# Performance work log

Measured on AMD Instinct MI355X. Metric: run time of the kernel, lower is better.

## Reference

```python
import jax, jax.numpy as jnp
import numpy as np

B = 1024
FEATS = [("sirna_gibbs_energy", 19), ("pssm_score", 1), ("gc_sterch", 1), ("sirna_second_percent", 2), ("sirna_second_energy", 2), ("tri_nt_percent", 64), ("di_nt_percent", 16), ("single_nt_percent", 4), ("gc_content", 1)]
DFF = 2048  # torch TransformerEncoderLayer default dim_feedforward


def _posenc(S, d):
    pos = jnp.arange(S, dtype=jnp.float32)[:, None]
    div = jnp.exp(jnp.arange(0, d, 2, dtype=jnp.float32) * (-np.log(10000.0) / d))
    pe = jnp.zeros((S, d), jnp.float32)
    pe = pe.at[:, 0::2].set(jnp.sin(pos * div))
    pe = pe.at[:, 1::2].set(jnp.cos(pos * div))
    return pe


def _ln(x, g, b):
    m = x.mean(-1, keepdims=True)
    v = ((x - m) ** 2).mean(-1, keepdims=True)
    return (x - m) * jax.lax.rsqrt(v + 1e-5) * g + b


def _encoder_layer(x, qkv_w, qkv_b, ow, ob, f1w, f1b, f2w, f2b, g1, b1, g2, b2, nhead):
    Bx, S, d = x.shape
    dh = d // nhead
    qkv = jnp.einsum('bsd,ed->bse', x, qkv_w) + qkv_b  # [B,S,3d]
    q, k, v = jnp.split(qkv, 3, axis=-1)
    sh = lambda t: t.reshape(Bx, S, nhead, dh).transpose(0, 2, 1, 3)  # [B,h,S,dh]
    q, k, v = sh(q), sh(k), sh(v)
    att = jax.nn.softmax(jnp.einsum('bhqd,bhkd->bhqk', q, k) / np.sqrt(dh).astype(np.float32), axis=-1)
    o = jnp.einsum('bhqk,bhkd->bhqd', att, v).transpose(0, 2, 1, 3).reshape(Bx, S, d)
    o = o @ ow.T + ob
    x = _ln(x + o, g1, b1)  # post-norm (norm_first=False default)
    h = jax.nn.relu(x @ f1w.T + f1b) @ f2w.T + f2b
    return _ln(x + h, g2, b2)


def _encoder(x, qkv_w, qkv_b, ow, ob, f1w, f1b, f2w, f2b, g1, b1, g2, b2, nhead):
    for i in range(qkv_w.shape[0]):
        x = _encoder_layer(x, qkv_w[i], qkv_b[i], ow[i], ob[i], f1w[i], f1b[i], f2w[i], f2b[i], g1[i], b1[i], g2[i], b2[i], nhead)
    return x


def setup_inputs():
    key = jax.random.key(0)
    ks = iter(jax.random.split(key, 128))
    inp = {}
    inp['rnafm_encode'] = jax.random.normal(next(ks), (B, 21, 640), jnp.float32)
    inp['rnafm_encode_mrna'] = jax.random.normal(next(ks), (B, 59, 640), jnp.float32)
    for name, n in FEATS:
        inp[name] = jax.random.normal(next(ks), (B, n, 1), jnp.float32)

    def xav(shape):
        fan_out, fan_in = shape[-2], shape[-1]
        std = np.sqrt(2.0 / (fan_in + fan_out)).astype(np.float32)
        return jax.random.normal(next(ks), shape, jnp.float32) * std

    def enc_params(prefix, L, d):
        inp[prefix + '_qkv_w'] = xav((L, 3 * d, d))
        inp[prefix + '_qkv_b'] = jnp.zeros((L, 3 * d), jnp.float32)
        inp[prefix + '_ow'] = xav((L, d, d))
        inp[prefix + '_ob'] = jnp.zeros((L, d), jnp.float32)
        inp[prefix + '_f1w'] = xav((L, DFF, d))
        inp[prefix + '_f1b'] = jnp.zeros((L, DFF), jnp.float32)
        inp[prefix + '_f2w'] = xav((L, d, DFF))
        inp[prefix + '_f2b'] = jnp.zeros((L, d), jnp.float32)
        inp[prefix + '_g1'] = jnp.ones((L, d), jnp.float32)
        inp[prefix + '_b1'] = jnp.zeros((L, d), jnp.float32)
        inp[prefix + '_g2'] = jnp.ones((L, d), jnp.float32)
        inp[prefix + '_b2'] = jnp.zeros((L, d), jnp.float32)

    inp['xmap1_w'] = xav((16, 640)); inp['xmap1_b'] = jnp.zeros(16, jnp.float32)
    enc_params('enc1', 4, 16)
    inp['ymap1_w'] = xav((4, 16)); inp['ymap1_b'] = jnp.zeros(4, jnp.float32)
    inp['xmap2_w'] = xav((8, 640)); inp['xmap2_b'] = jnp.zeros(8, jnp.float32)
    enc_params('enc2', 2, 8)
    inp['ymap2_w'] = xav((1, 8)); inp['ymap2_b'] = jnp.zeros(1, jnp.float32)
    inp['bn_g'] = jnp.ones(253, jnp.float32); inp['bn_b'] = jnp.zeros(253, jnp.float32)
    inp['d1w'] = xav((256, 253)); inp['d1b'] = jnp.zeros(256, jnp.float32)
    inp['d2w'] = xav((64, 256)); inp['d2b'] = jnp.zeros(64, jnp.float32)
    inp['d3w'] = xav((16, 64)); inp['d3b'] = jnp.zeros(16, jnp.float32)
    inp['d4w'] = xav((1, 16)); inp['d4b'] = jnp.zeros(1, jnp.float32)
    return inp


def _forward(rnafm_encode, rnafm_encode_mrna, feats,
             xmap1_w, xmap1_b, enc1, ymap1_w, ymap1_b,
             xmap2_w, xmap2_b, enc2, ymap2_w, ymap2_b,
             bn_g, bn_b, d1w, d1b, d2w, d2b, d3w, d3b, d4w, d4b):
    # siRNA branch: [B,21,640] -> [B,21,16] -> encoder(4 layers, 2 heads) -> [B,21,4]
    x = rnafm_encode @ xmap1_w.T + xmap1_b
    x = x + _posenc(21, 16)
    x = _encoder(x, *enc1, nhead=2)
    as_att = (x @ ymap1_w.T + ymap1_b).reshape(x.shape[0], -1)  # [B,84]
    # mRNA branch: [B,59,640] -> [B,59,8] -> encoder(2 layers, 1 head) -> [B,59,1]
    y = rnafm_encode_mrna @ xmap2_w.T + xmap2_b
    y = y + _posenc(59, 8)
    y = _encoder(y, *enc2, nhead=1)
    mrna_att = (y @ ymap2_w.T + ymap2_b).reshape(y.shape[0], -1)  # [B,59]
    other = jnp.concatenate([f[..., 0] for f in feats], axis=1)  # [B,110]
    cat = jnp.concatenate([as_att, mrna_att, other], axis=1)  # [B,253]
    # BatchNorm1d in eval mode (running_mean=0, running_var=1, eps=1e-5)
    h = cat * jax.lax.rsqrt(jnp.float32(1.0 + 1e-5)) * bn_g + bn_b
    h = jax.nn.leaky_relu(h @ d1w.T + d1b, 0.01)
    h = jax.nn.leaky_relu(h @ d2w.T + d2b, 0.01)
    h = jax.nn.leaky_relu(h @ d3w.T + d3b, 0.01)
    out = jax.nn.sigmoid(h @ d4w.T + d4b)
    return out[:, 0]


def reference(rnafm_encode, rnafm_encode_mrna, sirna_gibbs_energy, pssm_score, gc_sterch,
              sirna_second_percent, sirna_second_energy, tri_nt_percent, di_nt_percent,
              single_nt_percent, gc_content,
              xmap1_w, xmap1_b,
              enc1_qkv_w, enc1_qkv_b, enc1_ow, enc1_ob, enc1_f1w, enc1_f1b, enc1_f2w, enc1_f2b,
              enc1_g1, enc1_b1, enc1_g2, enc1_b2,
              ymap1_w, ymap1_b,
              xmap2_w, xmap2_b,
              enc2_qkv_w, enc2_qkv_b, enc2_ow, enc2_ob, enc2_f1w, enc2_f1b, enc2_f2w, enc2_f2b,
              enc2_g1, enc2_b1, enc2_g2, enc2_b2,
              ymap2_w, ymap2_b,
              bn_g, bn_b, d1w, d1b, d2w, d2b, d3w, d3b, d4w, d4b):
    feats = (sirna_gibbs_energy, pssm_score, gc_sterch, sirna_second_percent,
             sirna_second_energy, tri_nt_percent, di_nt_percent, single_nt_percent, gc_content)
    enc1 = (enc1_qkv_w, enc1_qkv_b, enc1_ow, enc1_ob, enc1_f1w, enc1_f1b, enc1_f2w, enc1_f2b,
            enc1_g1, enc1_b1, enc1_g2, enc1_b2)
    enc2 = (enc2_qkv_w, enc2_qkv_b, enc2_ow, enc2_ob, enc2_f1w, enc2_f1b, enc2_f2w, enc2_f2b,
            enc2_g1, enc2_b1, enc2_g2, enc2_b2)
    return _forward(rnafm_encode, rnafm_encode_mrna, feats,
                    xmap1_w, xmap1_b, enc1, ymap1_w, ymap1_b,
                    xmap2_w, xmap2_b, enc2, ymap2_w, ymap2_b,
                    bn_g, bn_b, d1w, d1b, d2w, d2b, d3w, d3b, d4w, d4b)
```

## Files before the change

kernel.cpp:

```cpp
#include <hip/hip_runtime.h>
#include <math.h>

#define NB 1024

typedef __bf16 mbf8 __attribute__((ext_vector_type(8)));
typedef float  mf4  __attribute__((ext_vector_type(4)));

union Pk { __bf16 h[4]; uint2 u2; };

__device__ __forceinline__ mf4 mfma16(mbf8 a, mbf8 b, mf4 c) {
  return __builtin_amdgcn_mfma_f32_16x16x32_bf16(a, b, c, 0, 0, 0);
}

__device__ __forceinline__ mbf8 ld_frag_f32(const float* p) {
  float4 u0 = *(const float4*)p;
  float4 u1 = *(const float4*)(p + 4);
  mbf8 v;
  v[0]=(__bf16)u0.x; v[1]=(__bf16)u0.y; v[2]=(__bf16)u0.z; v[3]=(__bf16)u0.w;
  v[4]=(__bf16)u1.x; v[5]=(__bf16)u1.y; v[6]=(__bf16)u1.z; v[7]=(__bf16)u1.w;
  return v;
}

__device__ __forceinline__ mbf8 ld_frag_f32_scaled(const float* p, float s) {
  float4 u0 = *(const float4*)p;
  float4 u1 = *(const float4*)(p + 4);
  mbf8 v;
  v[0]=(__bf16)(u0.x*s); v[1]=(__bf16)(u0.y*s); v[2]=(__bf16)(u0.z*s); v[3]=(__bf16)(u0.w*s);
  v[4]=(__bf16)(u1.x*s); v[5]=(__bf16)(u1.y*s); v[6]=(__bf16)(u1.z*s); v[7]=(__bf16)(u1.w*s);
  return v;
}

__device__ __forceinline__ mbf8 zero8() {
  mbf8 v;
  #pragma unroll
  for (int q = 0; q < 8; ++q) v[q] = (__bf16)0.f;
  return v;
}

__global__ __launch_bounds__(256) void prep_kernel(
    const float* __restrict__ xw1, const float* __restrict__ f1w1, const float* __restrict__ f2w1,
    const float* __restrict__ xw2, const float* __restrict__ f1w2, const float* __restrict__ f2w2,
    const float* __restrict__ d1w, const float* __restrict__ d2w, const float* __restrict__ d3w,
    __bf16* __restrict__ out)
{
  int idx = blockIdx.x * 256 + threadIdx.x;
  if (idx >= 693248) return;
  int which, local;
  if (idx < 10240)       { which = 0; local = idx; }
  else if (idx < 272384) { which = 1; local = idx - 10240; }
  else if (idx < 403456) { which = 2; local = idx - 272384; }
  else if (idx < 413696) { which = 3; local = idx - 403456; }
  else if (idx < 544768) { which = 4; local = idx - 413696; }
  else if (idx < 610304) { which = 5; local = idx - 544768; }
  else if (idx < 675840) { which = 6; local = idx - 610304; }
  else if (idx < 692224) { which = 7; local = idx - 675840; }
  else                   { which = 8; local = idx - 692224; }
  int tile = local >> 9, r = local & 511, lane = r >> 3, j = r & 7;
  int quad = lane >> 4, lm = lane & 15, khi = quad * 8 + j;
  float val = 0.f;
  switch (which) {
    case 0: { int k = tile*32 + khi; val = xw1[lm*640 + k]; } break;
    case 1: { int L = tile >> 7, nt = tile & 127, n = nt*16 + lm;
              val = (khi < 16) ? f1w1[(L*2048 + n)*16 + khi] : 0.f; } break;
    case 2: { int L = tile >> 6, ks = tile & 63, k = ks*32 + khi;
              val = f2w1[(L*16 + lm)*2048 + k]; } break;
    case 3: { int k = tile*32 + khi; val = (lm < 8) ? xw2[lm*640 + k] : 0.f; } break;
    case 4: { int L = tile >> 7, nt = tile & 127, n = nt*16 + lm;
              val = (khi < 8) ? f1w2[(L*2048 + n)*8 + khi] : 0.f; } break;
    case 5: { int L = tile >> 6, ks = tile & 63, k = ks*32 + khi;
              val = (lm < 8) ? f2w2[(L*8 + lm)*2048 + k] : 0.f; } break;
    case 6: { int nt = tile >> 3, ks = tile & 7, k = ks*32 + khi;
              val = (k < 253) ? d1w[(nt*16 + lm)*253 + k] : 0.f; } break;
    case 7: { int nt = tile >> 3, ks = tile & 7, k = ks*32 + khi;
              val = d2w[(nt*16 + lm)*256 + k]; } break;
    default:{ int ks = tile, k = ks*32 + khi;
              val = d3w[lm*64 + k]; } break;
  }
  out[idx] = (__bf16)val;
}

__device__ __forceinline__ void run_b1(int b, float* smem,
    const float* __restrict__ inp, const float* __restrict__ xb,
    const float* __restrict__ qw, const float* __restrict__ qb,
    const float* __restrict__ ow, const float* __restrict__ ob,
    const float* __restrict__ f1b, const float* __restrict__ f2b,
    const float* __restrict__ g1w, const float* __restrict__ b1w,
    const float* __restrict__ g2w, const float* __restrict__ b2w,
    const float* __restrict__ ymw, const float* __restrict__ ymb,
    const __bf16* __restrict__ xwB, const __bf16* __restrict__ w1B,
    const __bf16* __restrict__ w2B, float* __restrict__ outp)
{
  float* xs   = smem;
  float* ao   = smem + 420;
  float* pool = smem + 840;

  const int tid = threadIdx.x;
  const int w = tid >> 6, lane = tid & 63, quad = lane >> 4, lm = lane & 15;
  float* qkv = pool;
  __bf16* pbuf = (__bf16*)(pool + 1092);
  __bf16* hbuf = (__bf16*)pool;
  float* red = pool;
  const float* Ain = inp + (size_t)b * 21 * 640;

  mf4 pc0 = {0.f,0.f,0.f,0.f}, pc1 = {0.f,0.f,0.f,0.f};
  for (int i = 0; i < 5; ++i) {
    int ks = w*5 + i;
    mbf8 bv = *(const mbf8*)(xwB + (ks*64 + lane)*8);
    #pragma unroll
    for (int mt = 0; mt < 2; ++mt) {
      int row = mt*16 + lm; row = row > 20 ? 20 : row;
      mbf8 av = ld_frag_f32(Ain + row*640 + ks*32 + quad*8);
      if (mt == 0) pc0 = mfma16(av, bv, pc0); else pc1 = mfma16(av, bv, pc1);
    }
  }
  #pragma unroll
  for (int r = 0; r < 4; ++r) {
    red[((w*2+0)*16 + quad*4 + r)*17 + lm] = pc0[r];
    red[((w*2+1)*16 + quad*4 + r)*17 + lm] = pc1[r];
  }
  __syncthreads();
  {
    const float lf = -logf(10000.0f) / 16.0f;
    for (int idx = tid; idx < 336; idx += 256) {
      int t = idx >> 4, i = idx & 15, mt = t >> 4, tl = t & 15;
      float s = red[((0+mt)*16+tl)*17+i] + red[((2+mt)*16+tl)*17+i]
              + red[((4+mt)*16+tl)*17+i] + red[((6+mt)*16+tl)*17+i];
      float freq = expf((float)((i>>1)*2) * lf);
      float pe = (i & 1) ? cosf((float)t * freq) : sinf((float)t * freq);
      xs[t*20 + i] = s + xb[i] + pe;
    }
  }
  __syncthreads();

  for (int L = 0; L < 4; ++L) {
    for (int idx = tid; idx < 1008; idx += 256) {
      int s = idx / 48, e = idx % 48;
      const float* wr = qw + (L*48 + e)*16;
      float a = qb[L*48 + e];
      #pragma unroll
      for (int k = 0; k < 16; ++k) a += xs[s*20+k] * wr[k];
      qkv[s*52 + e] = a;
    }
    __syncthreads();

    {
      int h = w >> 1, mt = w & 1;
      __bf16* pb = pbuf + w*640;
      int tokq = mt*16 + lm; tokq = tokq > 20 ? 20 : tokq;
      mbf8 qf = zero8();
      if (quad == 0) qf = ld_frag_f32_scaled(qkv + tokq*52 + h*8, 0.35355339059327373f);
      float scr[2][4];
      #pragma unroll
      for (int nt = 0; nt < 2; ++nt) {
        int key = nt*16 + lm; key = key > 20 ? 20 : key;
        mbf8 kf = zero8();
        if (quad == 0) kf = ld_frag_f32(qkv + key*52 + 16 + h*8);
        mf4 z = {0.f,0.f,0.f,0.f};
        mf4 c = mfma16(qf, kf, z);
        int col = nt*16 + lm;
        #pragma unroll
        for (int r = 0; r < 4; ++r) scr[nt][r] = (col < 21) ? c[r] : -1e30f;
      }
      #pragma unroll
      for (int r = 0; r < 4; ++r) {
        float m = fmaxf(scr[0][r], scr[1][r]);
        m = fmaxf(m, __shfl_xor(m, 1)); m = fmaxf(m, __shfl_xor(m, 2));
        m = fmaxf(m, __shfl_xor(m, 4)); m = fmaxf(m, __shfl_xor(m, 8));
        float e0 = __expf(scr[0][r] - m), e1 = __expf(scr[1][r] - m);
        float s = e0 + e1;
        s += __shfl_xor(s, 1); s += __shfl_xor(s, 2);
        s += __shfl_xor(s, 4); s += __shfl_xor(s, 8);
        float inv = 1.f / s;
        scr[0][r] = e0 * inv; scr[1][r] = e1 * inv;
      }
      #pragma unroll
      for (int nt = 0; nt < 2; ++nt)
        #pragma unroll
        for (int r = 0; r < 4; ++r)
          pb[(quad*4 + r)*40 + nt*16 + lm] = (__bf16)scr[nt][r];
      mbf8 pf = *(const mbf8*)(pb + lm*40 + quad*8);
      mbf8 vf = zero8();
      #pragma unroll
      for (int j = 0; j < 8; ++j) {
        int k = quad*8 + j;
        vf[j] = (__bf16)((lm < 8 && k < 21) ? qkv[k*52 + 32 + h*8 + lm] : 0.f);
      }
      mf4 z = {0.f,0.f,0.f,0.f};
      mf4 c = mfma16(pf, vf, z);
      #pragma unroll
      for (int r = 0; r < 4; ++r) {
        int tok = mt*16 + quad*4 + r;
        if (tok < 21 && lm < 8) ao[tok*20 + h*8 + lm] = c[r];
      }
    }
    __syncthreads();

    for (int idx = tid; idx < 336; idx += 256) {
      int s = idx >> 4, i = idx & 15;
      const float* wr = ow + (L*16 + i)*16;
      float a = ob[L*16 + i];
      #pragma unroll
      for (int c = 0; c < 16; ++c) a += ao[s*20 + c] * wr[c];
      float v = xs[s*20 + i] + a;
      float m = v;
      m += __shfl_xor(m, 1); m += __shfl_xor(m, 2);
      m += __shfl_xor(m, 4); m += __shfl_xor(m, 8);
      m *= (1.f/16.f);
      float d = v - m;
      float va = d*d;
      va += __shfl_xor(va, 1); va += __shfl_xor(va, 2);
      va += __shfl_xor(va, 4); va += __shfl_xor(va, 8);
      va *= (1.f/16.f);
      xs[s*20 + i] = d * rsqrtf(va + 1e-5f) * g1w[L*16+i] + b1w[L*16+i];
    }
    __syncthreads();

    mbf8 xf0 = zero8(), xf1 = zero8();
    if (quad < 2) {
      int t0 = lm;
      int t1 = 16 + lm; if (t1 > 20) t1 = 20;
      xf0 = ld_frag_f32(xs + t0*20 + quad*8);
      xf1 = ld_frag_f32(xs + t1*20 + quad*8);
    }
    mf4 of0 = {0.f,0.f,0.f,0.f}, of1 = {0.f,0.f,0.f,0.f};
    const __bf16* w1L = w1B + (size_t)L*128*512;
    const __bf16* w2L = w2B + (size_t)L*64*512;
    const float* f1bL = f1b + L*2048;
    for (int ci = 0; ci < 8; ++ci) {
      #pragma unroll
      for (int u = 0; u < 4; ++u) {
        int ut = ci*16 + w*4 + u;
        mbf8 wa = *(const mbf8*)(w1L + (ut*64 + lane)*8);
        float4 bia = *(const float4*)(f1bL + ut*16 + quad*4);
        mf4 z = {0.f,0.f,0.f,0.f};
        mf4 c0 = mfma16(wa, xf0, z);
        mf4 c1 = mfma16(wa, xf1, z);
        Pk p0, p1;
        p0.h[0]=(__bf16)fmaxf(c0[0]+bia.x,0.f); p0.h[1]=(__bf16)fmaxf(c0[1]+bia.y,0.f);
        p0.h[2]=(__bf16)fmaxf(c0[2]+bia.z,0.f); p0.h[3]=(__bf16)fmaxf(c0[3]+bia.w,0.f);
        p1.h[0]=(__bf16)fmaxf(c1[0]+bia.x,0.f); p1.h[1]=(__bf16)fmaxf(c1[1]+bia.y,0.f);
        p1.h[2]=(__bf16)fmaxf(c1[2]+bia.z,0.f); p1.h[3]=(__bf16)fmaxf(c1[3]+bia.w,0.f);
        int colb = (ut & 15)*16 + quad*4;
        *(uint2*)(hbuf + lm*264 + colb)        = p0.u2;
        *(uint2*)(hbuf + (16 + lm)*264 + colb) = p1.u2;
      }
      #pragma unroll
      for (int kk = 0; kk < 2; ++kk) {
        int ksl = w*2 + kk;
        mbf8 wb = *(const mbf8*)(w2L + ((ci*8 + ksl)*64 + lane)*8);
        mbf8 a0 = *(const mbf8*)(hbuf + lm*264 + ksl*32 + quad*8);
        mbf8 a1 = *(const mbf8*)(hbuf + (16 + lm)*264 + ksl*32 + quad*8);
        of0 = mfma16(a0, wb, of0);
        of1 = mfma16(a1, wb, of1);
      }
    }
    __syncthreads();
    #pragma unroll
    for (int r = 0; r < 4; ++r) {
      red[((w*2+0)*16 + quad*4 + r)*17 + lm] = of0[r];
      red[((w*2+1)*16 + quad*4 + r)*17 + lm] = of1[r];
    }
    __syncthreads();
    for (int idx = tid; idx < 336; idx += 256) {
      int t = idx >> 4, i = idx & 15, mt = t >> 4, tl = t & 15;
      float s = red[((0+mt)*16+tl)*17+i] + red[((2+mt)*16+tl)*17+i]
              + red[((4+mt)*16+tl)*17+i] + red[((6+mt)*16+tl)*17+i];
      float v = xs[t*20 + i] + s + f2b[L*16 + i];
      float m = v;
      m += __shfl_xor(m, 1); m += __shfl_xor(m, 2);
      m += __shfl_xor(m, 4); m += __shfl_xor(m, 8);
      m *= (1.f/16.f);
      float d = v - m;
      float va = d*d;
      va += __shfl_xor(va, 1); va += __shfl_xor(va, 2);
      va += __shfl_xor(va, 4); va += __shfl_xor(va, 8);
      va *= (1.f/16.f);
      xs[t*20 + i] = d * rsqrtf(va + 1e-5f) * g2w[L*16+i] + b2w[L*16+i];
    }
    __syncthreads();
  }

  for (int idx = tid; idx < 84; idx += 256) {
    int s = idx >> 2, j = idx & 3;
    float a = ymb[j];
    #pragma unroll
    for (int k = 0; k < 16; ++k) a += xs[s*20 + k] * ymw[j*16 + k];
    outp[(size_t)b*84 + idx] = a;
  }
}

__device__ __forceinline__ void run_b2(int b, float* smem,
    const float* __restrict__ inp, const float* __restrict__ xb,
    const float* __restrict__ qw, const float* __restrict__ qb,
    const float* __restrict__ ow, const float* __restrict__ ob,
    const float* __restrict__ f1b, const float* __restrict__ f2b,
    const float* __restrict__ g1w, const float* __restrict__ b1w,
    const float* __restrict__ g2w, const float* __restrict__ b2w,
    const float* __restrict__ ymw, const float* __restrict__ ymb,
    const __bf16* __restrict__ xwB, const __bf16* __restrict__ w1B,
    const __bf16* __restrict__ w2B, float* __restrict__ outp)
{
  float* xs   = smem;
  float* ao   = smem + 708;
  float* pool = smem + 1416;

  const int tid = threadIdx.x;
  const int w = tid >> 6, lane = tid & 63, quad = lane >> 4, lm = lane & 15;
  float* qkv = pool;
  __bf16* pbuf = (__bf16*)(pool + 1652);
  __bf16* hbuf = (__bf16*)pool;
  float* red = pool;
  const float* Ain = inp + (size_t)b * 59 * 640;

  mf4 pc[4];
  #pragma unroll
  for (int mt = 0; mt < 4; ++mt) { mf4 z = {0.f,0.f,0.f,0.f}; pc[mt] = z; }
  for (int i = 0; i < 5; ++i) {
    int ks = w*5 + i;
    mbf8 bv = *(const mbf8*)(xwB + (ks*64 + lane)*8);
    #pragma unroll
    for (int mt = 0; mt < 4; ++mt) {
      int row = mt*16 + lm; row = row > 58 ? 58 : row;
      mbf8 av = ld_frag_f32(Ain + row*640 + ks*32 + quad*8);
      pc[mt] = mfma16(av, bv, pc[mt]);
    }
  }
  #pragma unroll
  for (int mt = 0; mt < 4; ++mt)
    #pragma unroll
    for (int r = 0; r < 4; ++r)
      red[((w*4+mt)*16 + quad*4 + r)*17 + lm] = pc[mt][r];
  __syncthreads();
  {
    const float lf = -logf(10000.0f) / 8.0f;
    for (int idx = tid; idx < 472; idx += 256) {
      int t = idx >> 3, i = idx & 7, mt = t >> 4, tl = t & 15;
      float s = red[((0*4+mt)*16+tl)*17+i] + red[((1*4+mt)*16+tl)*17+i]
              + red[((2*4+mt)*16+tl)*17+i] + red[((3*4+mt)*16+tl)*17+i];
      float freq = expf((float)((i>>1)*2) * lf);
      float pe = (i & 1) ? cosf((float)t * freq) : sinf((float)t * freq);
      xs[t*12 + i] = s + xb[i] + pe;
    }
  }
  __syncthreads();

  for (int L = 0; L < 2; ++L) {
    for (int idx = tid; idx < 1416; idx += 256) {
      int s = idx / 24, e = idx % 24;
      const float* wr = qw + (L*24 + e)*8;
      float a = qb[L*24 + e];
      #pragma unroll
      for (int k = 0; k < 8; ++k) a += xs[s*12+k] * wr[k];
      qkv[s*28 + e] = a;
    }
    __syncthreads();

    {
      __bf16* pb = pbuf + w*1152;
      int tokq = w*16 + lm; tokq = tokq > 58 ? 58 : tokq;
      mbf8 qf = zero8();
      if (quad == 0) qf = ld_frag_f32_scaled(qkv + tokq*28, 0.35355339059327373f);
      float scr[4][4];
      #pragma unroll
      for (int nt = 0; nt < 4; ++nt) {
        int key = nt*16 + lm; key = key > 58 ? 58 : key;
        mbf8 kf = zero8();
        if (quad == 0) kf = ld_frag_f32(qkv + key*28 + 8);
        mf4 z = {0.f,0.f,0.f,0.f};
        mf4 c = mfma16(qf, kf, z);
        int col = nt*16 + lm;
        #pragma unroll
        for (int r = 0; r < 4; ++r) scr[nt][r] = (col < 59) ? c[r] : -1e30f;
      }
      #pragma unroll
      for (int r = 0; r < 4; ++r) {
        float m = fmaxf(fmaxf(scr[0][r], scr[1][r]), fmaxf(scr[2][r], scr[3][r]));
        m = fmaxf(m, __shfl_xor(m, 1)); m = fmaxf(m, __shfl_xor(m, 2));
        m = fmaxf(m, __shfl_xor(m, 4)); m = fmaxf(m, __shfl_xor(m, 8));
        float e0 = __expf(scr[0][r] - m), e1 = __expf(scr[1][r] - m);
        float e2 = __expf(scr[2][r] - m), e3 = __expf(scr[3][r] - m);
        float s = (e0 + e1) + (e2 + e3);
        s += __shfl_xor(s, 1); s += __shfl_xor(s, 2);
        s += __shfl_xor(s, 4); s += __shfl_xor(s, 8);
        float inv = 1.f / s;
        scr[0][r] = e0 * inv; scr[1][r] = e1 * inv;
        scr[2][r] = e2 * inv; scr[3][r] = e3 * inv;
      }
      #pragma unroll
      for (int nt = 0; nt < 4; ++nt)
        #pragma unroll
        for (int r = 0; r < 4; ++r)
          pb[(quad*4 + r)*72 + nt*16 + lm] = (__bf16)scr[nt][r];
      mf4 acc = {0.f,0.f,0.f,0.f};
      #pragma unroll
      for (int kk = 0; kk < 2; ++kk) {
        mbf8 pf = *(const mbf8*)(pb + lm*72 + kk*32 + quad*8);
        mbf8 vf = zero8();
        #pragma unroll
        for (int j = 0; j < 8; ++j) {
          int k = kk*32 + quad*8 + j;
          vf[j] = (__bf16)((lm < 8 && k < 59) ? qkv[k*28 + 16 + lm] : 0.f);
        }
        acc = mfma16(pf, vf, acc);
      }
      #pragma unroll
      for (int r = 0; r < 4; ++r) {
        int tok = w*16 + quad*4 + r;
        if (tok < 59 && lm < 8) ao[tok*12 + lm] = acc[r];
      }
    }
    __syncthreads();

    for (int idx = tid; idx < 472; idx += 256) {
      int s = idx >> 3, i = idx & 7;
      const float* wr = ow + (L*8 + i)*8;
      float a = ob[L*8 + i];
      #pragma unroll
      for (int c = 0; c < 8; ++c) a += ao[s*12 + c] * wr[c];
      float v = xs[s*12 + i] + a;
      float m = v;
      m += __shfl_xor(m, 1); m += __shfl_xor(m, 2); m += __shfl_xor(m, 4);
      m *= 0.125f;
      float d = v - m;
      float va = d*d;
      va += __shfl_xor(va, 1); va += __shfl_xor(va, 2); va += __shfl_xor(va, 4);
      va *= 0.125f;
      xs[s*12 + i] = d * rsqrtf(va + 1e-5f) * g1w[L*8+i] + b1w[L*8+i];
    }
    __syncthreads();

    mbf8 xf[4];
    #pragma unroll
    for (int tt = 0; tt < 4; ++tt) {
      xf[tt] = zero8();
      if (quad == 0) {
        int tok = tt*16 + lm; if (tok > 58) tok = 58;
        xf[tt] = ld_frag_f32(xs + tok*12);
      }
    }
    mf4 of[4];
    #pragma unroll
    for (int mt = 0; mt < 4; ++mt) { mf4 z = {0.f,0.f,0.f,0.f}; of[mt] = z; }
    const __bf16* w1L = w1B + (size_t)L*128*512;
    const __bf16* w2L = w2B + (size_t)L*64*512;
    const float* f1bL = f1b + L*2048;
    for (int ci = 0; ci < 16; ++ci) {
      #pragma unroll
      for (int u = 0; u < 2; ++u) {
        int ut = ci*8 + w*2 + u;
        mbf8 wa = *(const mbf8*)(w1L + (ut*64 + lane)*8);
        float4 bia = *(const float4*)(f1bL + ut*16 + quad*4);
        int colb = (ut & 7)*16 + quad*4;
        #pragma unroll
        for (int tt = 0; tt < 4; ++tt) {
          mf4 z = {0.f,0.f,0.f,0.f};
          mf4 c = mfma16(wa, xf[tt], z);
          Pk p;
          p.h[0]=(__bf16)fmaxf(c[0]+bia.x,0.f); p.h[1]=(__bf16)fmaxf(c[1]+bia.y,0.f);
          p.h[2]=(__bf16)fmaxf(c[2]+bia.z,0.f); p.h[3]=(__bf16)fmaxf(c[3]+bia.w,0.f);
          *(uint2*)(hbuf + (tt*16 + lm)*136 + colb) = p.u2;
        }
      }
      {
        mbf8 wb = *(const mbf8*)(w2L + ((ci*4 + w)*64 + lane)*8);
        #pragma unroll
        for (int mt = 0; mt < 4; ++mt) {
          mbf8 ah = *(const mbf8*)(hbuf + (mt*16 + lm)*136 + w*32 + quad*8);
          of[mt] = mfma16(ah, wb, of[mt]);
        }
      }
    }
    __syncthreads();
    #pragma unroll
    for (int mt = 0; mt < 4; ++mt)
      #pragma unroll
      for (int r = 0; r < 4; ++r)
        red[((w*4+mt)*16 + quad*4 + r)*17 + lm] = of[mt][r];
    __syncthreads();
    for (int idx = tid; idx < 472; idx += 256) {
      int t = idx >> 3, i = idx & 7, mt = t >> 4, tl = t & 15;
      float s = red[((0*4+mt)*16+tl)*17+i] + red[((1*4+mt)*16+tl)*17+i]
              + red[((2*4+mt)*16+tl)*17+i] + red[((3*4+mt)*16+tl)*17+i];
      float v = xs[t*12 + i] + s + f2b[L*8 + i];
      float m = v;
      m += __shfl_xor(m, 1); m += __shfl_xor(m, 2); m += __shfl_xor(m, 4);
      m *= 0.125f;
      float d = v - m;
      float va = d*d;
      va += __shfl_xor(va, 1); va += __shfl_xor(va, 2); va += __shfl_xor(va, 4);
      va *= 0.125f;
      xs[t*12 + i] = d * rsqrtf(va + 1e-5f) * g2w[L*8+i] + b2w[L*8+i];
    }
    __syncthreads();
  }

  for (int s = tid; s < 59; s += 256) {
    float a = ymb[0];
    #pragma unroll
    for (int k = 0; k < 8; ++k) a += xs[s*12 + k] * ymw[k];
    outp[(size_t)b*59 + s] = a;
  }
}

__global__ __launch_bounds__(256) void enc_kernel(
    const float* __restrict__ inp1, const float* __restrict__ inp2,
    const float* __restrict__ xb1,
    const float* __restrict__ qw1, const float* __restrict__ qb1,
    const float* __restrict__ ow1, const float* __restrict__ ob1,
    const float* __restrict__ f1b1, const float* __restrict__ f2b1,
    const float* __restrict__ g1w1, const float* __restrict__ b1w1,
    const float* __restrict__ g2w1, const float* __restrict__ b2w1,
    const float* __restrict__ ymw1, const float* __restrict__ ymb1,
    const __bf16* __restrict__ xw1B, const __bf16* __restrict__ w1B1,
    const __bf16* __restrict__ w2B1,
    const float* __restrict__ xb2,
    const float* __restrict__ qw2, const float* __restrict__ qb2,
    const float* __restrict__ ow2, const float* __restrict__ ob2,
    const float* __restrict__ f1b2, const float* __restrict__ f2b2,
    const float* __restrict__ g1w2, const float* __restrict__ b1w2,
    const float* __restrict__ g2w2, const float* __restrict__ b2w2,
    const float* __restrict__ ymw2, const float* __restrict__ ymb2,
    const __bf16* __restrict__ xw2B, const __bf16* __restrict__ w1B2,
    const __bf16* __restrict__ w2B2,
    float* __restrict__ as_att, float* __restrict__ mrna)
{
  __shared__ __align__(16) float smem[5792];
  int bid = blockIdx.x;
  int b = bid >> 1;
  if ((bid & 1) == 0) {
    run_b1(b, smem, inp1, xb1, qw1, qb1, ow1, ob1, f1b1, f2b1,
           g1w1, b1w1, g2w1, b2w1, ymw1, ymb1, xw1B, w1B1, w2B1, as_att);
  } else {
    run_b2(b, smem, inp2, xb2, qw2, qb2, ow2, ob2, f1b2, f2b2,
           g1w2, b1w2, g2w2, b2w2, ymw2, ymb2, xw2B, w1B2, w2B2, mrna);
  }
}

__global__ __launch_bounds__(256) void mlp_kernel(
    const float* __restrict__ as_att, const float* __restrict__ mrna,
    const float* __restrict__ f_gibbs, const float* __restrict__ f_pssm,
    const float* __restrict__ f_gcs, const float* __restrict__ f_ssp,
    const float* __restrict__ f_sse, const float* __restrict__ f_tri,
    const float* __restrict__ f_di, const float* __restrict__ f_sgl,
    const float* __restrict__ f_gc,
    const float* __restrict__ bn_g, const float* __restrict__ bn_b,
    const float* __restrict__ d1b, const float* __restrict__ d2b,
    const float* __restrict__ d3b,
    const float* __restrict__ d4w, const float* __restrict__ d4b,
    const __bf16* __restrict__ d1B, const __bf16* __restrict__ d2B,
    const __bf16* __restrict__ d3B,
    float* __restrict__ outp)
{
  __shared__ __align__(16) float cat[16*268];
  __shared__ __align__(16) float h1[16*268];
  __shared__ __align__(16) float h2[16*68];
  __shared__ __align__(16) float h3[16*17];
  const int tid = threadIdx.x;
  const int bs  = blockIdx.x * 16;
  const int w = tid >> 6, lane = tid & 63, quad = lane >> 4, lm = lane & 15;
  const float bnscale = rsqrtf(1.0f + 1e-5f);

  for (int g = 0; g < 16; ++g) {
    int smp = bs + g;
    for (int j = tid; j < 253; j += 256) {
      float v;
      if (j < 84)       v = as_att[(size_t)smp*84 + j];
      else if (j < 143) v = mrna[(size_t)smp*59 + (j - 84)];
      else {
        int j2 = j - 143;
        if (j2 < 19)       v = f_gibbs[smp*19 + j2];
        else if (j2 < 20)  v = f_pssm[smp];
        else if (j2 < 21)  v = f_gcs[smp];
        else if (j2 < 23)  v = f_ssp[smp*2 + (j2-21)];
        else if (j2 < 25)  v = f_sse[smp*2 + (j2-23)];
        else if (j2 < 89)  v = f_tri[smp*64 + (j2-25)];
        else if (j2 < 105) v = f_di[smp*16 + (j2-89)];
        else if (j2 < 109) v = f_sgl[smp*4 + (j2-105)];
        else               v = f_gc[smp];
      }
      cat[g*268 + j] = v * bnscale * bn_g[j] + bn_b[j];
    }
  }
  if (tid < 48) { int g = tid / 3; cat[g*268 + 253 + tid % 3] = 0.f; }
  __syncthreads();

  {
    mf4 acc[4];
    #pragma unroll
    for (int q = 0; q < 4; ++q) { mf4 z = {0.f,0.f,0.f,0.f}; acc[q] = z; }
    for (int ks = 0; ks < 8; ++ks) {
      mbf8 af = ld_frag_f32(cat + lm*268 + ks*32 + quad*8);
      #pragma unroll
      for (int nt4 = 0; nt4 < 4; ++nt4) {
        int nt = w*4 + nt4;
        mbf8 bf = *(const mbf8*)(d1B + ((nt*8 + ks)*64 + lane)*8);
        acc[nt4] = mfma16(af, bf, acc[nt4]);
      }
    }
    #pragma unroll
    for (int nt4 = 0; nt4 < 4; ++nt4) {
      int n = (w*4 + nt4)*16 + lm;
      float bb = d1b[n];
      #pragma unroll
      for (int r = 0; r < 4; ++r) {
        float a = acc[nt4][r] + bb;
        h1[(quad*4 + r)*268 + n] = (a > 0.f) ? a : 0.01f * a;
      }
    }
  }
  __syncthreads();

  {
    mf4 acc = {0.f,0.f,0.f,0.f};
    for (int ks = 0; ks < 8; ++ks) {
      mbf8 af = ld_frag_f32(h1 + lm*268 + ks*32 + quad*8);
      mbf8 bf = *(const mbf8*)(d2B + ((w*8 + ks)*64 + lane)*8);
      acc = mfma16(af, bf, acc);
    }
    int n = w*16 + lm;
    float bb = d2b[n];
    #pragma unroll
    for (int r = 0; r < 4; ++r) {
      float a = acc[r] + bb;
      h2[(quad*4 + r)*68 + n] = (a > 0.f) ? a : 0.01f * a;
    }
  }
  __syncthreads();

  if (w == 0) {
    mf4 acc = {0.f,0.f,0.f,0.f};
    #pragma unroll
    for (int ks = 0; ks < 2; ++ks) {
      mbf8 af = ld_frag_f32(h2 + lm*68 + ks*32 + quad*8);
      mbf8 bf = *(const mbf8*)(d3B + (ks*64 + lane)*8);
      acc = mfma16(af, bf, acc);
    }
    float bb = d3b[lm];
    #pragma unroll
    for (int r = 0; r < 4; ++r) {
      float a = acc[r] + bb;
      h3[(quad*4 + r)*17 + lm] = (a > 0.f) ? a : 0.01f * a;
    }
  }
  __syncthreads();

  if (tid < 16) {
    float a = d4b[0];
    #pragma unroll
    for (int j = 0; j < 16; ++j) a += h3[tid*17 + j] * d4w[j];
    outp[bs + tid] = 1.f / (1.f + __expf(-a));
  }
}

extern "C" void kernel_launch(void* const* d_in, const int* in_sizes, int n_in,
                              void* d_out, int out_size, void* d_ws, size_t ws_size,
                              hipStream_t stream) {
  const float* rnafm   = (const float*)d_in[0];
  const float* rnafm_m = (const float*)d_in[1];
  const float* f_gibbs = (const float*)d_in[2];
  const float* f_pssm  = (const float*)d_in[3];
  const float* f_gcs   = (const float*)d_in[4];
  const float* f_ssp   = (const float*)d_in[5];
  const float* f_sse   = (const float*)d_in[6];
  const float* f_tri   = (const float*)d_in[7];
  const float* f_di    = (const float*)d_in[8];
  const float* f_sgl   = (const float*)d_in[9];
  const float* f_gc    = (const float*)d_in[10];
  const float* xmap1_w = (const float*)d_in[11];
  const float* xmap1_b = (const float*)d_in[12];
  const float* e1_qw   = (const float*)d_in[13];
  const float* e1_qb   = (const float*)d_in[14];
  const float* e1_ow   = (const float*)d_in[15];
  const float* e1_ob   = (const float*)d_in[16];
  const float* e1_f1w  = (const float*)d_in[17];
  const float* e1_f1b  = (const float*)d_in[18];
  const float* e1_f2w  = (const float*)d_in[19];
  const float* e1_f2b  = (const float*)d_in[20];
  const float* e1_g1   = (const float*)d_in[21];
  const float* e1_b1   = (const float*)d_in[22];
  const float* e1_g2   = (const float*)d_in[23];
  const float* e1_b2   = (const float*)d_in[24];
  const float* ymap1_w = (const float*)d_in[25];
  const float* ymap1_b = (const float*)d_in[26];
  const float* xmap2_w = (const float*)d_in[27];
  const float* xmap2_b = (const float*)d_in[28];
  const float* e2_qw   = (const float*)d_in[29];
  const float* e2_qb   = (const float*)d_in[30];
  const float* e2_ow   = (const float*)d_in[31];
  const float* e2_ob   = (const float*)d_in[32];
  const float* e2_f1w  = (const float*)d_in[33];
  const float* e2_f1b  = (const float*)d_in[34];
  const float* e2_f2w  = (const float*)d_in[35];
  const float* e2_f2b  = (const float*)d_in[36];
  const float* e2_g1   = (const float*)d_in[37];
  const float* e2_b1   = (const float*)d_in[38];
  const float* e2_g2   = (const float*)d_in[39];
  const float* e2_b2   = (const float*)d_in[40];
  const float* ymap2_w = (const float*)d_in[41];
  const float* ymap2_b = (const float*)d_in[42];
  const float* bn_g    = (const float*)d_in[43];
  const float* bn_b    = (const float*)d_in[44];
  const float* d1w     = (const float*)d_in[45];
  const float* d1b     = (const float*)d_in[46];
  const float* d2w     = (const float*)d_in[47];
  const float* d2b     = (const float*)d_in[48];
  const float* d3w     = (const float*)d_in[49];
  const float* d3b     = (const float*)d_in[50];
  const float* d4w     = (const float*)d_in[51];
  const float* d4b     = (const float*)d_in[52];

  float* as_att = (float*)d_ws;
  float* mrna   = (float*)((char*)d_ws + (size_t)NB*84*4);
  __bf16* bfb   = (__bf16*)((char*)d_ws + 585728);
  __bf16* xw1B  = bfb;
  __bf16* w1B1  = bfb + 10240;
  __bf16* w2B1  = bfb + 272384;
  __bf16* xw2B  = bfb + 403456;
  __bf16* w1B2  = bfb + 413696;
  __bf16* w2B2  = bfb + 544768;
  __bf16* d1B   = bfb + 610304;
  __bf16* d2B   = bfb + 675840;
  __bf16* d3B   = bfb + 692224;
  float* outp   = (float*)d_out;

  prep_kernel<<<2708, 256, 0, stream>>>(xmap1_w, e1_f1w, e1_f2w, xmap2_w, e2_f1w, e2_f2w,
                                        d1w, d2w, d3w, bfb);

  enc_kernel<<<2*NB, 256, 0, stream>>>(rnafm, rnafm_m,
      xmap1_b, e1_qw, e1_qb, e1_ow, e1_ob, e1_f1b, e1_f2b,
      e1_g1, e1_b1, e1_g2, e1_b2, ymap1_w, ymap1_b, xw1B, w1B1, w2B1,
      xmap2_b, e2_qw, e2_qb, e2_ow, e2_ob, e2_f1b, e2_f2b,
      e2_g1, e2_b1, e2_g2, e2_b2, ymap2_w, ymap2_b, xw2B, w1B2, w2B2,
      as_att, mrna);

  mlp_kernel<<<64, 256, 0, stream>>>(as_att, mrna,
      f_gibbs, f_pssm, f_gcs, f_ssp, f_sse, f_tri, f_di, f_sgl, f_gc,
      bn_g, bn_b, d1b, d2b, d3b, d4w, d4b, d1B, d2B, d3B, outp);
}
```

Before: 516.6 us.

## Use MFMA for QKV and output projections and pad FFN hidden buffer stride

```diff
diff --git a/kernel.cpp b/kernel.cpp
--- a/kernel.cpp
+++ b/kernel.cpp
@@ -41,10 +41,12 @@
     const float* __restrict__ xw1, const float* __restrict__ f1w1, const float* __restrict__ f2w1,
     const float* __restrict__ xw2, const float* __restrict__ f1w2, const float* __restrict__ f2w2,
     const float* __restrict__ d1w, const float* __restrict__ d2w, const float* __restrict__ d3w,
+    const float* __restrict__ qw1, const float* __restrict__ ow1,
+    const float* __restrict__ qw2, const float* __restrict__ ow2,
     __bf16* __restrict__ out)
 {
   int idx = blockIdx.x * 256 + threadIdx.x;
-  if (idx >= 693248) return;
+  if (idx >= 704512) return;
   int which, local;
   if (idx < 10240)       { which = 0; local = idx; }
   else if (idx < 272384) { which = 1; local = idx - 10240; }
@@ -54,7 +56,11 @@
   else if (idx < 610304) { which = 5; local = idx - 544768; }
   else if (idx < 675840) { which = 6; local = idx - 610304; }
   else if (idx < 692224) { which = 7; local = idx - 675840; }
-  else                   { which = 8; local = idx - 692224; }
+  else if (idx < 693248) { which = 8; local = idx - 692224; }
+  else if (idx < 699392) { which = 9; local = idx - 693248; }
+  else if (idx < 701440) { which = 10; local = idx - 699392; }
+  else if (idx < 703488) { which = 11; local = idx - 701440; }
+  else                   { which = 12; local = idx - 703488; }
   int tile = local >> 9, r = local & 511, lane = r >> 3, j = r & 7;
   int quad = lane >> 4, lm = lane & 15, khi = quad * 8 + j;
   float val = 0.f;
@@ -73,22 +79,30 @@
               val = (k < 253) ? d1w[(nt*16 + lm)*253 + k] : 0.f; } break;
     case 7: { int nt = tile >> 3, ks = tile & 7, k = ks*32 + khi;
               val = d2w[(nt*16 + lm)*256 + k]; } break;
-    default:{ int ks = tile, k = ks*32 + khi;
+    case 8: { int ks = tile, k = ks*32 + khi;
               val = d3w[lm*64 + k]; } break;
+    case 9: { int L = tile / 3, nt = tile % 3, n = nt*16 + lm;
+              val = (khi < 16) ? qw1[(L*48 + n)*16 + khi] : 0.f; } break;
+    case 10:{ int L = tile;
+              val = (khi < 16) ? ow1[(L*16 + lm)*16 + khi] : 0.f; } break;
+    case 11:{ int L = tile >> 1, nt = tile & 1, n = nt*16 + lm;
+              val = (n < 24 && khi < 8) ? qw2[(L*24 + n)*8 + khi] : 0.f; } break;
+    default:{ int L = tile;
+              val = (lm < 8 && khi < 8) ? ow2[(L*8 + lm)*8 + khi] : 0.f; } break;
   }
   out[idx] = (__bf16)val;
 }
 
 __device__ __forceinline__ void run_b1(int b, float* smem,
     const float* __restrict__ inp, const float* __restrict__ xb,
-    const float* __restrict__ qw, const float* __restrict__ qb,
-    const float* __restrict__ ow, const float* __restrict__ ob,
+    const float* __restrict__ qb, const float* __restrict__ ob,
     const float* __restrict__ f1b, const float* __restrict__ f2b,
     const float* __restrict__ g1w, const float* __restrict__ b1w,
     const float* __restrict__ g2w, const float* __restrict__ b2w,
     const float* __restrict__ ymw, const float* __restrict__ ymb,
     const __bf16* __restrict__ xwB, const __bf16* __restrict__ w1B,
-    const __bf16* __restrict__ w2B, float* __restrict__ outp)
+    const __bf16* __restrict__ w2B, const __bf16* __restrict__ qkvB,
+    const __bf16* __restrict__ owB, float* __restrict__ outp)
 {
   float* xs   = smem;
   float* ao   = smem + 420;
@@ -133,13 +147,28 @@
   __syncthreads();
 
   for (int L = 0; L < 4; ++L) {
-    for (int idx = tid; idx < 1008; idx += 256) {
-      int s = idx / 48, e = idx % 48;
-      const float* wr = qw + (L*48 + e)*16;
-      float a = qb[L*48 + e];
-      #pragma unroll
-      for (int k = 0; k < 16; ++k) a += xs[s*20+k] * wr[k];
-      qkv[s*52 + e] = a;
+    {
+      int mt = w & 1;
+      mbf8 axf = zero8();
+      if (quad < 2) {
+        int t = mt*16 + lm; if (t > 20) t = 20;
+        axf = ld_frag_f32(xs + t*20 + quad*8);
+      }
+      const float* qbL = qb + L*48;
+      int npass = (w < 2) ? 2 : 1;
+      for (int pass = 0; pass < npass; ++pass) {
+        int nt = (w < 2) ? pass*2 : 1;
+        mbf8 bf = *(const mbf8*)(qkvB + ((L*3 + nt)*512) + lane*8);
+        mf4 z = {0.f,0.f,0.f,0.f};
+        mf4 c = mfma16(axf, bf, z);
+        int e = nt*16 + lm;
+        float bias = qbL[e];
+        #pragma unroll
+        for (int r = 0; r < 4; ++r) {
+          int s = mt*16 + quad*4 + r;
+          if (s < 21) qkv[s*52 + e] = c[r] + bias;
+        }
+      }
     }
     __syncthreads();
 
@@ -195,23 +224,34 @@
     }
     __syncthreads();
 
-    for (int idx = tid; idx < 336; idx += 256) {
-      int s = idx >> 4, i = idx & 15;
-      const float* wr = ow + (L*16 + i)*16;
-      float a = ob[L*16 + i];
-      #pragma unroll
-      for (int c = 0; c < 16; ++c) a += ao[s*20 + c] * wr[c];
-      float v = xs[s*20 + i] + a;
-      float m = v;
-      m += __shfl_xor(m, 1); m += __shfl_xor(m, 2);
-      m += __shfl_xor(m, 4); m += __shfl_xor(m, 8);
-      m *= (1.f/16.f);
-      float d = v - m;
-      float va = d*d;
-      va += __shfl_xor(va, 1); va += __shfl_xor(va, 2);
-      va += __shfl_xor(va, 4); va += __shfl_xor(va, 8);
-      va *= (1.f/16.f);
-      xs[s*20 + i] = d * rsqrtf(va + 1e-5f) * g1w[L*16+i] + b1w[L*16+i];
+    if (w < 2) {
+      int mt = w;
+      mbf8 af = zero8();
+      if (quad < 2) {
+        int t = mt*16 + lm; if (t > 20) t = 20;
+        af = ld_frag_f32(ao + t*20 + quad*8);
+      }
+      mbf8 bf = *(const mbf8*)(owB + L*512 + lane*8);
+      mf4 z = {0.f,0.f,0.f,0.f};
+      mf4 c = mfma16(af, bf, z);
+      float obv = ob[L*16 + lm], gg = g1w[L*16 + lm], bb = b1w[L*16 + lm];
+      #pragma unroll
+      for (int r = 0; r < 4; ++r) {
+        int s = mt*16 + quad*4 + r;
+        int sc_ = s > 20 ? 20 : s;
+        float v = c[r] + obv + xs[sc_*20 + lm];
+        float m = v;
+        m += __shfl_xor(m, 1); m += __shfl_xor(m, 2);
+        m += __shfl_xor(m, 4); m += __shfl_xor(m, 8);
+        m *= (1.f/16.f);
+        float d = v - m;
+        float va = d*d;
+        va += __shfl_xor(va, 1); va += __shfl_xor(va, 2);
+        va += __shfl_xor(va, 4); va += __shfl_xor(va, 8);
+        va *= (1.f/16.f);
+        float o = d * rsqrtf(va + 1e-5f) * gg + bb;
+        if (s < 21) xs[s*20 + lm] = o;
+      }
     }
     __syncthreads();
 
@@ -241,15 +281,15 @@
         p1.h[0]=(__bf16)fmaxf(c1[0]+bia.x,0.f); p1.h[1]=(__bf16)fmaxf(c1[1]+bia.y,0.f);
         p1.h[2]=(__bf16)fmaxf(c1[2]+bia.z,0.f); p1.h[3]=(__bf16)fmaxf(c1[3]+bia.w,0.f);
         int colb = (ut & 15)*16 + quad*4;
-        *(uint2*)(hbuf + lm*264 + colb)        = p0.u2;
-        *(uint2*)(hbuf + (16 + lm)*264 + colb) = p1.u2;
+        *(uint2*)(hbuf + lm*268 + colb)        = p0.u2;
+        *(uint2*)(hbuf + (16 + lm)*268 + colb) = p1.u2;
       }
       #pragma unroll
       for (int kk = 0; kk < 2; ++kk) {
         int ksl = w*2 + kk;
         mbf8 wb = *(const mbf8*)(w2L + ((ci*8 + ksl)*64 + lane)*8);
-        mbf8 a0 = *(const mbf8*)(hbuf + lm*264 + ksl*32 + quad*8);
-        mbf8 a1 = *(const mbf8*)(hbuf + (16 + lm)*264 + ksl*32 + quad*8);
+        mbf8 a0 = *(const mbf8*)(hbuf + lm*268 + ksl*32 + quad*8);
+        mbf8 a1 = *(const mbf8*)(hbuf + (16 + lm)*268 + ksl*32 + quad*8);
         of0 = mfma16(a0, wb, of0);
         of1 = mfma16(a1, wb, of1);
       }
@@ -291,14 +331,14 @@
 
 __device__ __forceinline__ void run_b2(int b, float* smem,
     const float* __restrict__ inp, const float* __restrict__ xb,
-    const float* __restrict__ qw, const float* __restrict__ qb,
-    const float* __restrict__ ow, const float* __restrict__ ob,
+    const float* __restrict__ qb, const float* __restrict__ ob,
     const float* __restrict__ f1b, const float* __restrict__ f2b,
     const float* __restrict__ g1w, const float* __restrict__ b1w,
     const float* __restrict__ g2w, const float* __restrict__ b2w,
     const float* __restrict__ ymw, const float* __restrict__ ymb,
     const __bf16* __restrict__ xwB, const __bf16* __restrict__ w1B,
-    const __bf16* __restrict__ w2B, float* __restrict__ outp)
+    const __bf16* __restrict__ w2B, const __bf16* __restrict__ qkvB,
+    const __bf16* __restrict__ owB, float* __restrict__ outp)
 {
   float* xs   = smem;
   float* ao   = smem + 708;
@@ -345,13 +385,26 @@
   __syncthreads();
 
   for (int L = 0; L < 2; ++L) {
-    for (int idx = tid; idx < 1416; idx += 256) {
-      int s = idx / 24, e = idx % 24;
-      const float* wr = qw + (L*24 + e)*8;
-      float a = qb[L*24 + e];
-      #pragma unroll
-      for (int k = 0; k < 8; ++k) a += xs[s*12+k] * wr[k];
-      qkv[s*28 + e] = a;
+    {
+      int tok = w*16 + lm; if (tok > 58) tok = 58;
+      mbf8 axf = zero8();
+      if (quad == 0) axf = ld_frag_f32(xs + tok*12);
+      const float* qbL = qb + L*24;
+      #pragma unroll
+      for (int nt = 0; nt < 2; ++nt) {
+        mbf8 bf = *(const mbf8*)(qkvB + ((L*2 + nt)*512) + lane*8);
+        mf4 z = {0.f,0.f,0.f,0.f};
+        mf4 c = mfma16(axf, bf, z);
+        int e = nt*16 + lm;
+        if (e < 24) {
+          float bias = qbL[e];
+          #pragma unroll
+          for (int r = 0; r < 4; ++r) {
+            int s = w*16 + quad*4 + r;
+            if (s < 59) qkv[s*28 + e] = c[r] + bias;
+          }
+        }
+      }
     }
     __syncthreads();
 
@@ -411,21 +464,30 @@
     }
     __syncthreads();
 
-    for (int idx = tid; idx < 472; idx += 256) {
-      int s = idx >> 3, i = idx & 7;
-      const float* wr = ow + (L*8 + i)*8;
-      float a = ob[L*8 + i];
-      #pragma unroll
-      for (int c = 0; c < 8; ++c) a += ao[s*12 + c] * wr[c];
-      float v = xs[s*12 + i] + a;
-      float m = v;
-      m += __shfl_xor(m, 1); m += __shfl_xor(m, 2); m += __shfl_xor(m, 4);
-      m *= 0.125f;
-      float d = v - m;
-      float va = d*d;
-      va += __shfl_xor(va, 1); va += __shfl_xor(va, 2); va += __shfl_xor(va, 4);
-      va *= 0.125f;
-      xs[s*12 + i] = d * rsqrtf(va + 1e-5f) * g1w[L*8+i] + b1w[L*8+i];
+    {
+      int tok = w*16 + lm; if (tok > 58) tok = 58;
+      mbf8 af = zero8();
+      if (quad == 0) af = ld_frag_f32(ao + tok*12);
+      mbf8 bf = *(const mbf8*)(owB + L*512 + lane*8);
+      mf4 z = {0.f,0.f,0.f,0.f};
+      mf4 c = mfma16(af, bf, z);
+      int lm8 = lm & 7;
+      float obv = ob[L*8 + lm8], gg = g1w[L*8 + lm8], bb = b1w[L*8 + lm8];
+      #pragma unroll
+      for (int r = 0; r < 4; ++r) {
+        int s = w*16 + quad*4 + r;
+        int sc_ = s > 58 ? 58 : s;
+        float v = c[r] + obv + xs[sc_*12 + lm8];
+        float m = v;
+        m += __shfl_xor(m, 1); m += __shfl_xor(m, 2); m += __shfl_xor(m, 4);
+        m *= 0.125f;
+        float d = v - m;
+        float va = d*d;
+        va += __shfl_xor(va, 1); va += __shfl_xor(va, 2); va += __shfl_xor(va, 4);
+        va *= 0.125f;
+        float o = d * rsqrtf(va + 1e-5f) * gg + bb;
+        if (s < 59 && lm < 8) xs[s*12 + lm] = o;
+      }
     }
     __syncthreads();
 
@@ -458,14 +520,14 @@
           Pk p;
           p.h[0]=(__bf16)fmaxf(c[0]+bia.x,0.f); p.h[1]=(__bf16)fmaxf(c[1]+bia.y,0.f);
           p.h[2]=(__bf16)fmaxf(c[2]+bia.z,0.f); p.h[3]=(__bf16)fmaxf(c[3]+bia.w,0.f);
-          *(uint2*)(hbuf + (tt*16 + lm)*136 + colb) = p.u2;
+          *(uint2*)(hbuf + (tt*16 + lm)*140 + colb) = p.u2;
         }
       }
       {
         mbf8 wb = *(const mbf8*)(w2L + ((ci*4 + w)*64 + lane)*8);
         #pragma unroll
         for (int mt = 0; mt < 4; ++mt) {
-          mbf8 ah = *(const mbf8*)(hbuf + (mt*16 + lm)*136 + w*32 + quad*8);
+          mbf8 ah = *(const mbf8*)(hbuf + (mt*16 + lm)*140 + w*32 + quad*8);
           of[mt] = mfma16(ah, wb, of[mt]);
         }
       }
@@ -505,34 +567,34 @@
 __global__ __launch_bounds__(256) void enc_kernel(
     const float* __restrict__ inp1, const float* __restrict__ inp2,
     const float* __restrict__ xb1,
-    const float* __restrict__ qw1, const float* __restrict__ qb1,
-    const float* __restrict__ ow1, const float* __restrict__ ob1,
+    const float* __restrict__ qb1, const float* __restrict__ ob1,
     const float* __restrict__ f1b1, const float* __restrict__ f2b1,
     const float* __restrict__ g1w1, const float* __restrict__ b1w1,
     const float* __restrict__ g2w1, const float* __restrict__ b2w1,
     const float* __restrict__ ymw1, const float* __restrict__ ymb1,
     const __bf16* __restrict__ xw1B, const __bf16* __restrict__ w1B1,
-    const __bf16* __restrict__ w2B1,
+    const __bf16* __restrict__ w2B1, const __bf16* __restrict__ qkvB1,
+    const __bf16* __restrict__ owB1,
     const float* __restrict__ xb2,
-    const float* __restrict__ qw2, const float* __restrict__ qb2,
-    const float* __restrict__ ow2, const float* __restrict__ ob2,
+    const float* __restrict__ qb2, const float* __restrict__ ob2,
     const float* __restrict__ f1b2, const float* __restrict__ f2b2,
     const float* __restrict__ g1w2, const float* __restrict__ b1w2,
     const float* __restrict__ g2w2, const float* __restrict__ b2w2,
     const float* __restrict__ ymw2, const float* __restrict__ ymb2,
     const __bf16* __restrict__ xw2B, const __bf16* __restrict__ w1B2,
-    const __bf16* __restrict__ w2B2,
+    const __bf16* __restrict__ w2B2, const __bf16* __restrict__ qkvB2,
+    const __bf16* __restrict__ owB2,
     float* __restrict__ as_att, float* __restrict__ mrna)
 {
-  __shared__ __align__(16) float smem[5792];
+  __shared__ __align__(16) float smem[5896];
   int bid = blockIdx.x;
   int b = bid >> 1;
   if ((bid & 1) == 0) {
-    run_b1(b, smem, inp1, xb1, qw1, qb1, ow1, ob1, f1b1, f2b1,
-           g1w1, b1w1, g2w1, b2w1, ymw1, ymb1, xw1B, w1B1, w2B1, as_att);
+    run_b1(b, smem, inp1, xb1, qb1, ob1, f1b1, f2b1,
+           g1w1, b1w1, g2w1, b2w1, ymw1, ymb1, xw1B, w1B1, w2B1, qkvB1, owB1, as_att);
   } else {
-    run_b2(b, smem, inp2, xb2, qw2, qb2, ow2, ob2, f1b2, f2b2,
-           g1w2, b1w2, g2w2, b2w2, ymw2, ymb2, xw2B, w1B2, w2B2, mrna);
+    run_b2(b, smem, inp2, xb2, qb2, ob2, f1b2, f2b2,
+           g1w2, b1w2, g2w2, b2w2, ymw2, ymb2, xw2B, w1B2, w2B2, qkvB2, owB2, mrna);
   }
 }
 
@@ -721,16 +783,20 @@
   __bf16* d1B   = bfb + 610304;
   __bf16* d2B   = bfb + 675840;
   __bf16* d3B   = bfb + 692224;
+  __bf16* qkvB1 = bfb + 693248;
+  __bf16* owB1  = bfb + 699392;
+  __bf16* qkvB2 = bfb + 701440;
+  __bf16* owB2  = bfb + 703488;
   float* outp   = (float*)d_out;
 
-  prep_kernel<<<2708, 256, 0, stream>>>(xmap1_w, e1_f1w, e1_f2w, xmap2_w, e2_f1w, e2_f2w,
-                                        d1w, d2w, d3w, bfb);
+  prep_kernel<<<2752, 256, 0, stream>>>(xmap1_w, e1_f1w, e1_f2w, xmap2_w, e2_f1w, e2_f2w,
+                                        d1w, d2w, d3w, e1_qw, e1_ow, e2_qw, e2_ow, bfb);
 
   enc_kernel<<<2*NB, 256, 0, stream>>>(rnafm, rnafm_m,
-      xmap1_b, e1_qw, e1_qb, e1_ow, e1_ob, e1_f1b, e1_f2b,
-      e1_g1, e1_b1, e1_g2, e1_b2, ymap1_w, ymap1_b, xw1B, w1B1, w2B1,
-      xmap2_b, e2_qw, e2_qb, e2_ow, e2_ob, e2_f1b, e2_f2b,
-      e2_g1, e2_b1, e2_g2, e2_b2, ymap2_w, ymap2_b, xw2B, w1B2, w2B2,
+      xmap1_b, e1_qb, e1_ob, e1_f1b, e1_f2b,
+      e1_g1, e1_b1, e1_g2, e1_b2, ymap1_w, ymap1_b, xw1B, w1B1, w2B1, qkvB1, owB1,
+      xmap2_b, e2_qb, e2_ob, e2_f1b, e2_f2b,
+      e2_g1, e2_b1, e2_g2, e2_b2, ymap2_w, ymap2_b, xw2B, w1B2, w2B2, qkvB2, owB2,
       as_att, mrna);
 
   mlp_kernel<<<64, 256, 0, stream>>>(as_att, mrna,
```

Measured after the change: 591.5 us. 14.5% more time.
